# Optimization experiments

Hardware: AMD Instinct MI355X
Metric: run time of the kernel (lower is better)

Reference implementation:

```python
import jax, jax.numpy as jnp
import numpy as np

N_NODES = 100000
N_EDGES = 320000
N_GRAPHS = 4096
HID = 256
NUM_FEAT = 28


def setup_inputs() -> dict:
    key = jax.random.key(0)
    ks = jax.random.split(key, 20)
    inp = {}
    inp['x'] = jax.random.normal(ks[0], (N_NODES, NUM_FEAT), dtype=jnp.float32)
    inp['edge_index'] = jax.random.randint(ks[1], (2, N_EDGES), 0, N_NODES, dtype=jnp.int64)
    inp['batch'] = jnp.sort(jax.random.randint(ks[2], (N_NODES,), 0, N_GRAPHS, dtype=jnp.int64))
    def lin(k, out_d, in_d, scale=None):
        s = scale if scale is not None else 1.0 / np.sqrt(in_d)
        return jax.random.uniform(k, (out_d, in_d), jnp.float32, -s, s)
    # GraphConv layer l: W_rel (neighbor aggregate), b_rel, W_root (self)
    dims = [(HID, NUM_FEAT), (HID, HID), (HID, HID), (HID, HID)]
    for i, (o, d) in enumerate(dims, 1):
        inp[f'W{i}_rel'] = lin(ks[2 + 3 * i], o, d)
        inp[f'b{i}_rel'] = jnp.zeros((o,), jnp.float32)
        inp[f'W{i}_root'] = lin(ks[3 + 3 * i], o, d)
    inp['fc1_w'] = lin(ks[15], HID, 4 * HID)
    inp['fc1_b'] = jnp.zeros((HID,), jnp.float32)
    inp['fc2_w'] = lin(ks[16], HID, HID)
    inp['fc2_b'] = jnp.zeros((HID,), jnp.float32)
    inp['fc3_w'] = lin(ks[17], HID, HID)
    inp['fc3_b'] = jnp.zeros((HID,), jnp.float32)
    inp['fc4_w'] = lin(ks[18], 1, HID)
    inp['fc4_b'] = jnp.zeros((1,), jnp.float32)
    return inp


def _graph_conv(x, src, dst, W_rel, b_rel, W_root):
    # PyG GraphConv (aggr='add'): out = lin_rel(sum_{j->i} x_j) + lin_root(x_i)
    agg = jax.ops.segment_sum(x[src], dst, num_segments=N_NODES)  # [N, d]
    return agg @ W_rel.T + b_rel + x @ W_root.T


def reference(x, edge_index, batch,
              W1_rel, b1_rel, W1_root, W2_rel, b2_rel, W2_root,
              W3_rel, b3_rel, W3_root, W4_rel, b4_rel, W4_root,
              fc1_w, fc1_b, fc2_w, fc2_b, fc3_w, fc3_b, fc4_w, fc4_b):
    src, dst = edge_index[0], edge_index[1]
    x1 = jax.nn.relu(_graph_conv(x, src, dst, W1_rel, b1_rel, W1_root))
    x2 = jax.nn.relu(_graph_conv(x1, src, dst, W2_rel, b2_rel, W2_root))
    x3 = jax.nn.relu(_graph_conv(x2, src, dst, W3_rel, b3_rel, W3_root))
    x4 = jax.nn.relu(_graph_conv(x3, src, dst, W4_rel, b4_rel, W4_root))
    h = jnp.concatenate([x1, x2, x3, x4], axis=-1)  # [N, 4*HID]
    # global mean pool over graphs
    sums = jax.ops.segment_sum(h, batch, num_segments=N_GRAPHS)  # [G, 4*HID]
    cnts = jax.ops.segment_sum(jnp.ones((h.shape[0],), h.dtype), batch, num_segments=N_GRAPHS)
    g = sums / jnp.maximum(cnts, 1.0)[:, None]
    g = jax.nn.relu(g @ fc1_w.T + fc1_b)
    g = jax.nn.relu(g @ fc2_w.T + fc2_b)
    g = jax.nn.relu(g @ fc3_w.T + fc3_b)
    out = g @ fc4_w.T + fc4_b  # [G, 1]
    return out.reshape(-1)
```

## Files before the change

### kernel.cpp

```cpp
#include <hip/hip_runtime.h>
#include <hip/hip_bf16.h>
#include <cstdio>

#define HID 256

using short8  = __attribute__((ext_vector_type(8))) short;
using floatx4 = __attribute__((ext_vector_type(4))) float;

typedef const unsigned int __attribute__((address_space(1)))* as1_cuintp;
typedef unsigned int __attribute__((address_space(3)))* as3_uintp;

__device__ inline unsigned short bf16_rn(float x) {
    unsigned u = __float_as_uint(x);
    return (unsigned short)((u + 0x7FFFu + ((u >> 16) & 1u)) >> 16);
}
__device__ inline float bf2f(unsigned short u) {
    return __uint_as_float(((unsigned)u) << 16);
}

__global__ void marker_k(float* __restrict__ out, int n, float v) {
    int i = blockIdx.x * blockDim.x + threadIdx.x;
    if (i < n) out[i] = v;
}

__global__ void detect64_k(const unsigned* __restrict__ eiw, int E,
                           const unsigned* __restrict__ bw, int Nh,
                           int* __restrict__ any_nonzero) {
    int total = E + Nh;
    unsigned loc = 0;
    for (int i = blockIdx.x * blockDim.x + threadIdx.x; i < total;
         i += gridDim.x * blockDim.x) {
        loc |= (i < E) ? eiw[2 * i + 1] : bw[2 * (i - E) + 1];
    }
    if (loc) atomicOr(any_nonzero, 1);
}

__global__ void norm_idx_k(const int* __restrict__ src, int* __restrict__ dst,
                           int n, const int* __restrict__ any_nonzero) {
    int is64 = (any_nonzero[0] == 0);
    for (int i = blockIdx.x * blockDim.x + threadIdx.x; i < n;
         i += gridDim.x * blockDim.x) {
        dst[i] = is64 ? src[2 * i] : src[i];
    }
}

__global__ void pool_bounds_k(const int* __restrict__ batch, int N, int G,
                              int* __restrict__ starts) {
    int g = blockIdx.x * blockDim.x + threadIdx.x;
    if (g > G) return;
    int lo = 0, hi = N;
    while (lo < hi) {
        int mid = (lo + hi) >> 1;
        if (batch[mid] < g) lo = mid + 1; else hi = mid;
    }
    starts[g] = lo;
}

__global__ void deg_count_k(const int* __restrict__ ei, int E, int N,
                            int* __restrict__ deg) {
    int e = blockIdx.x * blockDim.x + threadIdx.x;
    if (e >= E) return;
    int s = ei[e];
    int d = ei[E + e];
    if ((unsigned)s >= (unsigned)N || (unsigned)d >= (unsigned)N) return;
    atomicAdd(&deg[d], 1);
}

#define SCAN_BLK 256

__global__ __launch_bounds__(SCAN_BLK) void scan_a_k(const int* __restrict__ deg,
                                                     int* __restrict__ bsum, int N) {
    __shared__ int red[SCAN_BLK];
    int i = blockIdx.x * SCAN_BLK + threadIdx.x;
    int v = (i < N) ? deg[i] : 0;
    red[threadIdx.x] = v;
    __syncthreads();
#pragma unroll
    for (int off = SCAN_BLK / 2; off > 0; off >>= 1) {
        if (threadIdx.x < off) red[threadIdx.x] += red[threadIdx.x + off];
        __syncthreads();
    }
    if (threadIdx.x == 0) bsum[blockIdx.x] = red[0];
}

__global__ __launch_bounds__(1024) void scan_b_k(int* __restrict__ bsum, int nb) {
    __shared__ int tsum[1024];
    int t = threadIdx.x;
    int v = (t < nb) ? bsum[t] : 0;
    tsum[t] = v;
    __syncthreads();
    for (int off = 1; off < 1024; off <<= 1) {
        int u = (t >= off) ? tsum[t - off] : 0;
        __syncthreads();
        tsum[t] += u;
        __syncthreads();
    }
    if (t < nb) bsum[t] = tsum[t] - v;
}

__global__ __launch_bounds__(SCAN_BLK) void scan_c_k(const int* __restrict__ deg,
                                                     const int* __restrict__ bsum,
                                                     int* __restrict__ row_ptr, int N) {
    __shared__ int tsum[SCAN_BLK];
    int t = threadIdx.x;
    int i = blockIdx.x * SCAN_BLK + t;
    int v = (i < N) ? deg[i] : 0;
    tsum[t] = v;
    __syncthreads();
    for (int off = 1; off < SCAN_BLK; off <<= 1) {
        int u = (t >= off) ? tsum[t - off] : 0;
        __syncthreads();
        tsum[t] += u;
        __syncthreads();
    }
    if (i <= N) row_ptr[i] = tsum[t] - v + bsum[blockIdx.x];
}

__global__ __launch_bounds__(1024) void scan_rowptr_k(const int* __restrict__ deg,
                                                      int* __restrict__ row_ptr, int N) {
    __shared__ int tsum[1024];
    int t = threadIdx.x;
    int chunk = (N + 1023) / 1024;
    int lo = t * chunk;
    int hi = min(lo + chunk, N);
    int s = 0;
    for (int i = lo; i < hi; i++) s += deg[i];
    tsum[t] = s;
    __syncthreads();
    for (int off = 1; off < 1024; off <<= 1) {
        int v = (t >= off) ? tsum[t - off] : 0;
        __syncthreads();
        tsum[t] += v;
        __syncthreads();
    }
    int run = (t == 0) ? 0 : tsum[t - 1];
    for (int i = lo; i < hi; i++) { row_ptr[i] = run; run += deg[i]; }
    if (hi >= N && lo <= N) row_ptr[N] = run;
}

__global__ void fill_csr_k(const int* __restrict__ ei, int E, int N,
                           const int* __restrict__ row_ptr, int* __restrict__ cursor,
                           int* __restrict__ esrc) {
    int e = blockIdx.x * blockDim.x + threadIdx.x;
    if (e >= E) return;
    int s = ei[e];
    int d = ei[E + e];
    if ((unsigned)s >= (unsigned)N || (unsigned)d >= (unsigned)N) return;
    int pos = atomicAdd(&cursor[d], 1);
    esrc[row_ptr[d] + pos] = s;
}

__global__ void gather28_k(const float* __restrict__ x, const int* __restrict__ row_ptr,
                           const int* __restrict__ esrc, float* __restrict__ Q28, int N) {
    int gid = blockIdx.x * blockDim.x + threadIdx.x;
    int node = gid >> 5;
    if (node >= N) return;
    int lane = gid & 31;
    if (lane >= 28) return;
    int s = row_ptr[node], e = row_ptr[node + 1];
    float acc = 0.f;
    for (int i = s; i < e; i++) {
        int src = esrc[i];
        acc += x[(size_t)src * 28 + lane];
    }
    Q28[(size_t)node * 28 + lane] = acc;
}

__global__ void gather256_k(const float* __restrict__ P, const int* __restrict__ row_ptr,
                            const int* __restrict__ esrc, float* __restrict__ Q, int N) {
    int gid = blockIdx.x * blockDim.x + threadIdx.x;
    int node = gid >> 6;
    if (node >= N) return;
    int lane = gid & 63;
    int s = row_ptr[node], e = row_ptr[node + 1];
    float4 acc = make_float4(0.f, 0.f, 0.f, 0.f);
    for (int i = s; i < e; i++) {
        int src = esrc[i];
        float4 v = *(const float4*)(P + (size_t)src * HID + lane * 4);
        acc.x += v.x; acc.y += v.y; acc.z += v.z; acc.w += v.w;
    }
    *(float4*)(Q + (size_t)node * HID + lane * 4) = acc;
}

__global__ __launch_bounds__(256) void l1_fused_k(
    const float* __restrict__ x, const float* __restrict__ agg,
    const float* __restrict__ Wrel, const float* __restrict__ Wroot,
    const float* __restrict__ bias, float* __restrict__ out, int M) {
    __shared__ float As[64][28];
    __shared__ float Xs[64][28];
    int t = threadIdx.x;
    int n0 = blockIdx.x * 64;
    float wrel[28], wroot[28];
#pragma unroll
    for (int k = 0; k < 28; k++) {
        wrel[k]  = Wrel[t * 28 + k];
        wroot[k] = Wroot[t * 28 + k];
    }
    float b = bias[t];
    for (int idx = t; idx < 64 * 28; idx += 256) {
        int r = idx / 28;
        int c = idx - r * 28;
        int gr = n0 + r;
        As[r][c] = (gr < M) ? agg[(size_t)gr * 28 + c] : 0.f;
        Xs[r][c] = (gr < M) ? x[(size_t)gr * 28 + c] : 0.f;
    }
    __syncthreads();
    int nmax = min(64, M - n0);
    for (int n = 0; n < nmax; n++) {
        float acc = b;
#pragma unroll
        for (int k4 = 0; k4 < 28; k4 += 4) {
            float4 a  = *(const float4*)&As[n][k4];
            float4 xx = *(const float4*)&Xs[n][k4];
            acc += a.x * wrel[k4] + a.y * wrel[k4 + 1] + a.z * wrel[k4 + 2] + a.w * wrel[k4 + 3];
            acc += xx.x * wroot[k4] + xx.y * wroot[k4 + 1] + xx.z * wroot[k4 + 2] + xx.w * wroot[k4 + 3];
        }
        out[(size_t)(n0 + n) * HID + t] = fmaxf(acc, 0.f);
    }
}

__global__ void wsplit6_k(const float* W0, const float* W1, const float* W2,
                          const float* W3, const float* W4, const float* W5,
                          unsigned short* __restrict__ out_hl, int n) {
    int i = blockIdx.x * blockDim.x + threadIdx.x;
    if (i >= n) return;
    const float* W = (blockIdx.y == 0) ? W0 : (blockIdx.y == 1) ? W1 :
                     (blockIdx.y == 2) ? W2 : (blockIdx.y == 3) ? W3 :
                     (blockIdx.y == 4) ? W4 : W5;
    unsigned short* o = out_hl + (size_t)blockIdx.y * 131072;
    float a = W[i];
    unsigned short h = bf16_rn(a);
    unsigned short lo = bf16_rn(a - bf2f(h));
    int col = i >> 8;
    int k   = i & 255;
    int ch  = k >> 5;
    int sg  = (k >> 3) & 3;
    int e   = k & 7;
    int gp  = sg ^ ((col >> 1) & 3);
    size_t base = (size_t)ch * 16384 + (size_t)col * 32 + gp * 8 + e;
    o[base] = h;
    o[base + 8192] = lo;
}

#define LSTR 40

__global__ __launch_bounds__(256) void gemm_strip_mfma_k(
    const float* __restrict__ Q, const unsigned short* __restrict__ Wr_hl,
    float* __restrict__ P, const unsigned short* __restrict__ Wo_hl,
    const float* __restrict__ bias, int M) {
    __shared__ __attribute__((aligned(16))) unsigned short Ah[64 * LSTR];
    __shared__ __attribute__((aligned(16))) unsigned short Al[64 * LSTR];
    __shared__ __attribute__((aligned(16))) unsigned short Wbuf[8192];
    int t = threadIdx.x;
    int brow = blockIdx.x * 64;
    int w = t >> 6;
    int l = t & 63;

    floatx4 acc[4][4];
#pragma unroll
    for (int i = 0; i < 4; i++)
#pragma unroll
        for (int j = 0; j < 4; j++) acc[i][j] = (floatx4){0.f, 0.f, 0.f, 0.f};

    int srow = t >> 2;
    int sg   = t & 3;

    for (int ch = 0; ch < 16; ch++) {
        int phase2 = (ch >= 8);
        const float* A = phase2 ? P : Q;
        const unsigned short* Whl = phase2 ? Wo_hl : Wr_hl;
        int kbase = (ch & 7) * 32;

        {
            const char* wg = (const char*)(Whl + (size_t)(ch & 7) * 16384) + w * 4096;
            char* ld = (char*)Wbuf + w * 4096;
#pragma unroll
            for (int i = 0; i < 4; i++) {
                __builtin_amdgcn_global_load_lds(
                    (as1_cuintp)(const void*)(wg + i * 1024 + l * 16),
                    (as3_uintp)(void*)(ld + i * 1024),
                    16, 0, 0);
            }
        }
        {
            int gr = brow + srow;
            float v[8];
            if (gr < M) {
                float4 u0 = *(const float4*)(A + (size_t)gr * HID + kbase + sg * 8);
                float4 u1 = *(const float4*)(A + (size_t)gr * HID + kbase + sg * 8 + 4);
                v[0] = u0.x; v[1] = u0.y; v[2] = u0.z; v[3] = u0.w;
                v[4] = u1.x; v[5] = u1.y; v[6] = u1.z; v[7] = u1.w;
            } else {
#pragma unroll
                for (int j = 0; j < 8; j++) v[j] = 0.f;
            }
            union { unsigned short us[8]; short8 v8; } hh, ll;
#pragma unroll
            for (int j = 0; j < 8; j++) {
                unsigned short h = bf16_rn(v[j]);
                float hf = __uint_as_float(((unsigned)h) << 16);
                hh.us[j] = h;
                ll.us[j] = bf16_rn(v[j] - hf);
            }
            int base = srow * LSTR + sg * 8;
            *(short8*)(Ah + base) = hh.v8;
            *(short8*)(Al + base) = ll.v8;
        }
        __syncthreads();

        int frow = l & 15;
        int fg   = l >> 4;
        short8 ahf[4], alf[4], wf[4];
#pragma unroll
        for (int rt = 0; rt < 4; rt++) {
            int base = (rt * 16 + frow) * LSTR + fg * 8;
            ahf[rt] = *(short8*)(Ah + base);
            alf[rt] = *(short8*)(Al + base);
        }
#pragma unroll
        for (int ct = 0; ct < 4; ct++) {
            int col = w * 64 + ct * 16 + frow;
            int gp = fg ^ ((col >> 1) & 3);
            wf[ct] = *(short8*)(Wbuf + col * 32 + gp * 8);
        }
        asm volatile("s_waitcnt lgkmcnt(0)" ::: "memory");
        __builtin_amdgcn_sched_barrier(0);
        {
            const char* wg = (const char*)(Whl + (size_t)(ch & 7) * 16384 + 8192) + w * 4096;
            char* ld = (char*)Wbuf + w * 4096;
#pragma unroll
            for (int i = 0; i < 4; i++) {
                __builtin_amdgcn_global_load_lds(
                    (as1_cuintp)(const void*)(wg + i * 1024 + l * 16),
                    (as3_uintp)(void*)(ld + i * 1024),
                    16, 0, 0);
            }
        }
        __builtin_amdgcn_s_setprio(1);
#pragma unroll
        for (int rt = 0; rt < 4; rt++)
#pragma unroll
            for (int ct = 0; ct < 4; ct++) {
                acc[rt][ct] = __builtin_amdgcn_mfma_f32_16x16x32_bf16(
                    ahf[rt], wf[ct], acc[rt][ct], 0, 0, 0);
                acc[rt][ct] = __builtin_amdgcn_mfma_f32_16x16x32_bf16(
                    alf[rt], wf[ct], acc[rt][ct], 0, 0, 0);
            }
        __builtin_amdgcn_s_setprio(0);
        asm volatile("s_waitcnt vmcnt(0)" ::: "memory");
        __builtin_amdgcn_sched_barrier(0);
#pragma unroll
        for (int ct = 0; ct < 4; ct++) {
            int col = w * 64 + ct * 16 + frow;
            int gp = fg ^ ((col >> 1) & 3);
            wf[ct] = *(short8*)(Wbuf + col * 32 + gp * 8);
        }
        __builtin_amdgcn_s_setprio(1);
#pragma unroll
        for (int rt = 0; rt < 4; rt++)
#pragma unroll
            for (int ct = 0; ct < 4; ct++)
                acc[rt][ct] = __builtin_amdgcn_mfma_f32_16x16x32_bf16(
                    ahf[rt], wf[ct], acc[rt][ct], 0, 0, 0);
        __builtin_amdgcn_s_setprio(0);
        __syncthreads();
    }

#pragma unroll
    for (int ct = 0; ct < 4; ct++) {
        int gc = w * 64 + ct * 16 + (l & 15);
        float bs = bias[gc];
#pragma unroll
        for (int rt = 0; rt < 4; rt++) {
            floatx4 a = acc[rt][ct];
#pragma unroll
            for (int r = 0; r < 4; r++) {
                int gr = brow + rt * 16 + (l >> 4) * 4 + r;
                if (gr < M)
                    P[(size_t)gr * HID + gc] = fmaxf(a[r] + bs, 0.f);
            }
        }
    }
}

__global__ __launch_bounds__(256) void pool_slice_k(const float* __restrict__ xl,
                                                    const int* __restrict__ starts,
                                                    float* __restrict__ gslice, int N) {
    int g = blockIdx.x;
    int t = threadIdx.x;
    int s = starts[g], e = starts[g + 1];
    s = max(0, min(s, N));
    e = max(s, min(e, N));
    float a = 0.f;
    for (int n = s; n < e; n++) a += xl[(size_t)n * HID + t];
    float inv = 1.f / (float)max(e - s, 1);
    gslice[(size_t)g * 1024 + t] = a * inv;
}

#define BM 64
#define BN 64
#define BK 32
#define LP 68

__global__ __launch_bounds__(256) void gemm_dual_k(
    const float* __restrict__ A1, int lda1, const float* __restrict__ W1,
    const float* __restrict__ A2, int lda2, const float* __restrict__ W2,
    const float* __restrict__ bias, float* __restrict__ out, int ldout,
    int M, int K1, int K2, int relu) {
    __shared__ float As[BK][LP];
    __shared__ float Ws[BK][LP];
    int t = threadIdx.x;
    int brow = blockIdx.x * BM;
    int bcol = blockIdx.y * BN;
    int tx = t & 15, ty = t >> 4;
    float acc[4][4] = {{0.f}};
    int Ktot = K1 + K2;
    int srow = t >> 3;
    int sk4 = (t & 7) << 2;

    for (int kk = 0; kk < Ktot; kk += BK) {
        int phase2 = (kk >= K1);
        const float* A = phase2 ? A2 : A1;
        const float* W = phase2 ? W2 : W1;
        int lda = phase2 ? lda2 : lda1;
        int ldw = phase2 ? K2 : K1;
        int kbase = phase2 ? (kk - K1) : kk;
#pragma unroll
        for (int i = 0; i < 2; i++) {
            int r = srow + i * 32;
            int gr = brow + r;
            float4 v = make_float4(0.f, 0.f, 0.f, 0.f);
            if (gr < M) v = *(const float4*)(A + (size_t)gr * lda + kbase + sk4);
            As[sk4 + 0][r] = v.x; As[sk4 + 1][r] = v.y;
            As[sk4 + 2][r] = v.z; As[sk4 + 3][r] = v.w;
            float4 w = *(const float4*)(W + (size_t)(bcol + r) * ldw + kbase + sk4);
            Ws[sk4 + 0][r] = w.x; Ws[sk4 + 1][r] = w.y;
            Ws[sk4 + 2][r] = w.z; Ws[sk4 + 3][r] = w.w;
        }
        __syncthreads();
#pragma unroll
        for (int k = 0; k < BK; k++) {
            float4 a = *(const float4*)&As[k][ty << 2];
            float4 w = *(const float4*)&Ws[k][tx << 2];
            float av[4] = {a.x, a.y, a.z, a.w};
            float wv[4] = {w.x, w.y, w.z, w.w};
#pragma unroll
            for (int i = 0; i < 4; i++)
#pragma unroll
                for (int j = 0; j < 4; j++)
                    acc[i][j] = fmaf(av[i], wv[j], acc[i][j]);
        }
        __syncthreads();
    }
#pragma unroll
    for (int i = 0; i < 4; i++) {
        int gr = brow + (ty << 2) + i;
        if (gr >= M) continue;
#pragma unroll
        for (int j = 0; j < 4; j++) {
            int gc = bcol + (tx << 2) + j;
            float v = acc[i][j] + bias[gc];
            if (relu) v = fmaxf(v, 0.f);
            out[(size_t)gr * ldout + gc] = v;
        }
    }
}

__global__ void fc4_k(const float* __restrict__ in, const float* __restrict__ w,
                      const float* __restrict__ b, float* __restrict__ out, int M) {
    int gid = blockIdx.x * blockDim.x + threadIdx.x;
    int row = gid >> 6;
    if (row >= M) return;
    int lane = gid & 63;
    float4 v  = *(const float4*)(in + (size_t)row * HID + lane * 4);
    float4 ww = *(const float4*)(w + lane * 4);
    float acc = v.x * ww.x + v.y * ww.y + v.z * ww.z + v.w * ww.w;
#pragma unroll
    for (int off = 32; off; off >>= 1) acc += __shfl_down(acc, off);
    if (lane == 0) out[row] = acc + b[0];
}

extern "C" void kernel_launch(void* const* d_in, const int* in_sizes, int n_in,
                              void* d_out, int out_size, void* d_ws, size_t ws_size,
                              hipStream_t stream) {
    const int N = in_sizes[0] / 28;
    const int E = in_sizes[1] / 2;
    const int G = out_size;

    const float* x        = (const float*)d_in[0];
    const int*   ei_raw   = (const int*)d_in[1];
    const int*   b_raw    = (const int*)d_in[2];
    const float* W1_rel  = (const float*)d_in[3];
    const float* b1      = (const float*)d_in[4];
    const float* W1_root = (const float*)d_in[5];
    const float* W2_rel  = (const float*)d_in[6];
    const float* b2      = (const float*)d_in[7];
    const float* W2_root = (const float*)d_in[8];
    const float* W3_rel  = (const float*)d_in[9];
    const float* b3      = (const float*)d_in[10];
    const float* W3_root = (const float*)d_in[11];
    const float* W4_rel  = (const float*)d_in[12];
    const float* b4      = (const float*)d_in[13];
    const float* W4_root = (const float*)d_in[14];
    const float* fc1_w = (const float*)d_in[15];
    const float* fc1_b = (const float*)d_in[16];
    const float* fc2_w = (const float*)d_in[17];
    const float* fc2_b = (const float*)d_in[18];
    const float* fc3_w = (const float*)d_in[19];
    const float* fc3_b = (const float*)d_in[20];
    const float* fc4_w = (const float*)d_in[21];
    const float* fc4_b = (const float*)d_in[22];
    float* out = (float*)d_out;

    size_t fN  = (size_t)N * HID;
    size_t off_P      = 0;
    size_t off_Q      = off_P + fN;
    size_t off_gpool  = off_Q + fN;
    size_t off_t1     = off_gpool + (size_t)G * 1024;
    size_t off_t2     = off_t1 + (size_t)G * HID;
    size_t off_ei     = off_t2 + (size_t)G * HID;
    size_t off_batch  = off_ei + (size_t)2 * E;
    size_t off_starts = off_batch + (size_t)N;
    size_t off_flag   = off_starts + (size_t)(G + 1);
    size_t off_deg    = off_flag + 1;
    size_t off_cur    = off_deg + (size_t)N;
    size_t off_rowp   = off_cur + (size_t)N;
    size_t off_bsum   = off_rowp + (size_t)(N + 1);
    size_t off_esrc   = off_bsum + 1024;
    size_t off_wsplit = (off_esrc + (size_t)E + 3) & ~(size_t)3;
    size_t need = (off_wsplit + 393216 + 16) * 4;

    if (ws_size < need) {
        fprintf(stderr, "[kernel_launch] ws too small: ws=%zu need=%zu\n", ws_size, need);
        marker_k<<<(G + 255) / 256, 256, 0, stream>>>(out, G, (float)(ws_size >> 20));
        return;
    }

    float* wsf   = (float*)d_ws;
    float* P     = wsf + off_P;
    float* Q     = wsf + off_Q;
    float* gpool = wsf + off_gpool;
    float* t1    = wsf + off_t1;
    float* t2    = wsf + off_t2;
    int* nei     = (int*)(wsf + off_ei);
    int* nbatch  = (int*)(wsf + off_batch);
    int* starts  = (int*)(wsf + off_starts);
    int* flag    = (int*)(wsf + off_flag);
    int* deg     = (int*)(wsf + off_deg);
    int* cursor  = (int*)(wsf + off_cur);
    int* row_ptr = (int*)(wsf + off_rowp);
    int* bsum    = (int*)(wsf + off_bsum);
    int* esrc    = (int*)(wsf + off_esrc);
    unsigned short* wsplit = (unsigned short*)(wsf + off_wsplit);

    hipMemsetAsync(flag, 0, sizeof(int), stream);
    detect64_k<<<1024, 256, 0, stream>>>((const unsigned*)ei_raw, E,
                                         (const unsigned*)b_raw, N / 2, flag);
    norm_idx_k<<<1024, 256, 0, stream>>>(ei_raw, nei, 2 * E, flag);
    norm_idx_k<<<512, 256, 0, stream>>>(b_raw, nbatch, N, flag);

    pool_bounds_k<<<(G + 1 + 255) / 256, 256, 0, stream>>>(nbatch, N, G, starts);

    hipMemsetAsync(deg, 0, 2 * (size_t)N * sizeof(int), stream);
    deg_count_k<<<(E + 255) / 256, 256, 0, stream>>>(nei, E, N, deg);
    int nb = (N + 1 + SCAN_BLK - 1) / SCAN_BLK;
    if (nb <= 1024) {
        scan_a_k<<<nb, SCAN_BLK, 0, stream>>>(deg, bsum, N);
        scan_b_k<<<1, 1024, 0, stream>>>(bsum, nb);
        scan_c_k<<<nb, SCAN_BLK, 0, stream>>>(deg, bsum, row_ptr, N);
    } else {
        scan_rowptr_k<<<1, 1024, 0, stream>>>(deg, row_ptr, N);
    }
    fill_csr_k<<<(E + 255) / 256, 256, 0, stream>>>(nei, E, N, row_ptr, cursor, esrc);

    wsplit6_k<<<dim3((65536 + 255) / 256, 6), 256, 0, stream>>>(
        W2_rel, W2_root, W3_rel, W3_root, W4_rel, W4_root, wsplit, 65536);

    int nstrips = (N + 63) / 64;

    gather28_k<<<((size_t)N * 32 + 255) / 256, 256, 0, stream>>>(x, row_ptr, esrc, Q, N);
    l1_fused_k<<<nstrips, 256, 0, stream>>>(x, Q, W1_rel, W1_root, b1, P, N);
    pool_slice_k<<<G, 256, 0, stream>>>(P, starts, gpool + 0, N);

    const float* bb[3] = {b2, b3, b4};
    for (int l = 0; l < 3; l++) {
        gather256_k<<<((size_t)N * 64 + 255) / 256, 256, 0, stream>>>(P, row_ptr, esrc, Q, N);
        gemm_strip_mfma_k<<<nstrips, 256, 0, stream>>>(
            Q, wsplit + (size_t)(2 * l) * 131072,
            P, wsplit + (size_t)(2 * l + 1) * 131072, bb[l], N);
        pool_slice_k<<<G, 256, 0, stream>>>(P, starts, gpool + 256 * (l + 1), N);
    }

    dim3 gdimG(G / BM, HID / BN);
    gemm_dual_k<<<gdimG, 256, 0, stream>>>(gpool, 1024, fc1_w, nullptr, 0, nullptr,
                                           fc1_b, t1, HID, G, 1024, 0, 1);
    gemm_dual_k<<<gdimG, 256, 0, stream>>>(t1, HID, fc2_w, nullptr, 0, nullptr,
                                           fc2_b, t2, HID, G, HID, 0, 1);
    gemm_dual_k<<<gdimG, 256, 0, stream>>>(t2, HID, fc3_w, nullptr, 0, nullptr,
                                           fc3_b, t1, HID, G, HID, 0, 1);
    fc4_k<<<(G * 64 + 255) / 256, 256, 0, stream>>>(t1, fc4_w, fc4_b, out, G);
}
```

Measured before the change: 954.0 us.

## Run first GraphConv layer on MFMA with split-bf16 and padded 32-wide inputs

Replaces the scalar FMA first-layer kernel with an MFMA kernel that pads the 28-feature inputs and aggregates to 32 columns. It splits activations and weights into bf16 hi/lo parts (three products) to keep near-fp32 accuracy. It adds a padding kernel and a weight-split kernel, plus extra workspace for the padded arrays. The aim is to cut the compute and register-heavy scalar loop of the old layer-1 kernel, at the cost of an extra pass over x and slightly different rounding.

```diff
diff --git a/kernel.cpp b/kernel.cpp
--- a/kernel.cpp
+++ b/kernel.cpp
@@ -150,20 +150,29 @@
     esrc[row_ptr[d] + pos] = s;
 }
 
+__global__ void pad_x_k(const float* __restrict__ x, float* __restrict__ X32, int N) {
+    int i = blockIdx.x * blockDim.x + threadIdx.x;
+    if (i >= N * 32) return;
+    int node = i >> 5;
+    int lane = i & 31;
+    X32[i] = (lane < 28) ? x[(size_t)node * 28 + lane] : 0.f;
+}
+
 __global__ void gather28_k(const float* __restrict__ x, const int* __restrict__ row_ptr,
-                           const int* __restrict__ esrc, float* __restrict__ Q28, int N) {
+                           const int* __restrict__ esrc, float* __restrict__ Q32, int N) {
     int gid = blockIdx.x * blockDim.x + threadIdx.x;
     int node = gid >> 5;
     if (node >= N) return;
     int lane = gid & 31;
-    if (lane >= 28) return;
-    int s = row_ptr[node], e = row_ptr[node + 1];
     float acc = 0.f;
-    for (int i = s; i < e; i++) {
-        int src = esrc[i];
-        acc += x[(size_t)src * 28 + lane];
-    }
-    Q28[(size_t)node * 28 + lane] = acc;
+    if (lane < 28) {
+        int s = row_ptr[node], e = row_ptr[node + 1];
+        for (int i = s; i < e; i++) {
+            int src = esrc[i];
+            acc += x[(size_t)src * 28 + lane];
+        }
+    }
+    Q32[(size_t)node * 32 + lane] = acc;
 }
 
 __global__ void gather256_k(const float* __restrict__ P, const int* __restrict__ row_ptr,
@@ -180,43 +189,6 @@
         acc.x += v.x; acc.y += v.y; acc.z += v.z; acc.w += v.w;
     }
     *(float4*)(Q + (size_t)node * HID + lane * 4) = acc;
-}
-
-__global__ __launch_bounds__(256) void l1_fused_k(
-    const float* __restrict__ x, const float* __restrict__ agg,
-    const float* __restrict__ Wrel, const float* __restrict__ Wroot,
-    const float* __restrict__ bias, float* __restrict__ out, int M) {
-    __shared__ float As[64][28];
-    __shared__ float Xs[64][28];
-    int t = threadIdx.x;
-    int n0 = blockIdx.x * 64;
-    float wrel[28], wroot[28];
-#pragma unroll
-    for (int k = 0; k < 28; k++) {
-        wrel[k]  = Wrel[t * 28 + k];
-        wroot[k] = Wroot[t * 28 + k];
-    }
-    float b = bias[t];
-    for (int idx = t; idx < 64 * 28; idx += 256) {
-        int r = idx / 28;
-        int c = idx - r * 28;
-        int gr = n0 + r;
-        As[r][c] = (gr < M) ? agg[(size_t)gr * 28 + c] : 0.f;
-        Xs[r][c] = (gr < M) ? x[(size_t)gr * 28 + c] : 0.f;
-    }
-    __syncthreads();
-    int nmax = min(64, M - n0);
-    for (int n = 0; n < nmax; n++) {
-        float acc = b;
-#pragma unroll
-        for (int k4 = 0; k4 < 28; k4 += 4) {
-            float4 a  = *(const float4*)&As[n][k4];
-            float4 xx = *(const float4*)&Xs[n][k4];
-            acc += a.x * wrel[k4] + a.y * wrel[k4 + 1] + a.z * wrel[k4 + 2] + a.w * wrel[k4 + 3];
-            acc += xx.x * wroot[k4] + xx.y * wroot[k4 + 1] + xx.z * wroot[k4 + 2] + xx.w * wroot[k4 + 3];
-        }
-        out[(size_t)(n0 + n) * HID + t] = fmaxf(acc, 0.f);
-    }
 }
 
 __global__ void wsplit6_k(const float* W0, const float* W1, const float* W2,
@@ -242,7 +214,165 @@
     o[base + 8192] = lo;
 }
 
+__global__ void wsplit1_k(const float* __restrict__ W0, const float* __restrict__ W1,
+                          unsigned short* __restrict__ o) {
+    int i = blockIdx.x * blockDim.x + threadIdx.x;
+    if (i >= 2 * 8192) return;
+    int m   = i >> 13;
+    int r   = i & 8191;
+    int col = r >> 5;
+    int k   = r & 31;
+    const float* W = m ? W1 : W0;
+    float a = (k < 28) ? W[col * 28 + k] : 0.f;
+    unsigned short h = bf16_rn(a);
+    unsigned short lo = bf16_rn(a - bf2f(h));
+    int sg = (k >> 3) & 3;
+    int e  = k & 7;
+    int gp = sg ^ ((col >> 1) & 3);
+    size_t base = (size_t)m * 16384 + (size_t)col * 32 + gp * 8 + e;
+    o[base] = h;
+    o[base + 8192] = lo;
+}
+
 #define LSTR 40
+
+__global__ __launch_bounds__(256) void l1_mfma_k(
+    const float* __restrict__ Q32, const unsigned short* __restrict__ Wrel_hl,
+    const float* __restrict__ X32, const unsigned short* __restrict__ Wroot_hl,
+    const float* __restrict__ bias, float* __restrict__ P, int M) {
+    __shared__ __attribute__((aligned(16))) unsigned short Ah[64 * LSTR];
+    __shared__ __attribute__((aligned(16))) unsigned short Al[64 * LSTR];
+    __shared__ __attribute__((aligned(16))) unsigned short Wbuf[8192];
+    int t = threadIdx.x;
+    int brow = blockIdx.x * 64;
+    int w = t >> 6;
+    int l = t & 63;
+
+    floatx4 acc[4][4];
+#pragma unroll
+    for (int i = 0; i < 4; i++)
+#pragma unroll
+        for (int j = 0; j < 4; j++) acc[i][j] = (floatx4){0.f, 0.f, 0.f, 0.f};
+
+    int srow = t >> 2;
+    int sg   = t & 3;
+
+#pragma unroll
+    for (int ch = 0; ch < 2; ch++) {
+        const float* A = ch ? X32 : Q32;
+        const unsigned short* Whl = ch ? Wroot_hl : Wrel_hl;
+
+        {
+            const char* wg = (const char*)Whl + w * 4096;
+            char* ld = (char*)Wbuf + w * 4096;
+#pragma unroll
+            for (int i = 0; i < 4; i++) {
+                __builtin_amdgcn_global_load_lds(
+                    (as1_cuintp)(const void*)(wg + i * 1024 + l * 16),
+                    (as3_uintp)(void*)(ld + i * 1024),
+                    16, 0, 0);
+            }
+        }
+        {
+            int gr = brow + srow;
+            float v[8];
+            if (gr < M) {
+                float4 u0 = *(const float4*)(A + (size_t)gr * 32 + sg * 8);
+                float4 u1 = *(const float4*)(A + (size_t)gr * 32 + sg * 8 + 4);
+                v[0] = u0.x; v[1] = u0.y; v[2] = u0.z; v[3] = u0.w;
+                v[4] = u1.x; v[5] = u1.y; v[6] = u1.z; v[7] = u1.w;
+            } else {
+#pragma unroll
+                for (int j = 0; j < 8; j++) v[j] = 0.f;
+            }
+            union { unsigned short us[8]; short8 v8; } hh, ll;
+#pragma unroll
+            for (int j = 0; j < 8; j++) {
+                unsigned short h = bf16_rn(v[j]);
+                float hf = bf2f(h);
+                hh.us[j] = h;
+                ll.us[j] = bf16_rn(v[j] - hf);
+            }
+            int base = srow * LSTR + sg * 8;
+            *(short8*)(Ah + base) = hh.v8;
+            *(short8*)(Al + base) = ll.v8;
+        }
+        __syncthreads();
+
+        int frow = l & 15;
+        int fg   = l >> 4;
+        short8 ahf[4], alf[4], wf[4];
+#pragma unroll
+        for (int rt = 0; rt < 4; rt++) {
+            int base = (rt * 16 + frow) * LSTR + fg * 8;
+            ahf[rt] = *(short8*)(Ah + base);
+            alf[rt] = *(short8*)(Al + base);
+        }
+#pragma unroll
+        for (int ct = 0; ct < 4; ct++) {
+            int col = w * 64 + ct * 16 + frow;
+            int gp = fg ^ ((col >> 1) & 3);
+            wf[ct] = *(short8*)(Wbuf + col * 32 + gp * 8);
+        }
+        asm volatile("s_waitcnt lgkmcnt(0)" ::: "memory");
+        __builtin_amdgcn_sched_barrier(0);
+        {
+            const char* wg = (const char*)(Whl + 8192) + w * 4096;
+            char* ld = (char*)Wbuf + w * 4096;
+#pragma unroll
+            for (int i = 0; i < 4; i++) {
+                __builtin_amdgcn_global_load_lds(
+                    (as1_cuintp)(const void*)(wg + i * 1024 + l * 16),
+                    (as3_uintp)(void*)(ld + i * 1024),
+                    16, 0, 0);
+            }
+        }
+        __builtin_amdgcn_s_setprio(1);
+#pragma unroll
+        for (int rt = 0; rt < 4; rt++)
+#pragma unroll
+            for (int ct = 0; ct < 4; ct++) {
+                acc[rt][ct] = __builtin_amdgcn_mfma_f32_16x16x32_bf16(
+                    ahf[rt], wf[ct], acc[rt][ct], 0, 0, 0);
+                acc[rt][ct] = __builtin_amdgcn_mfma_f32_16x16x32_bf16(
+                    alf[rt], wf[ct], acc[rt][ct], 0, 0, 0);
+            }
+        __builtin_amdgcn_s_setprio(0);
+        asm volatile("s_waitcnt vmcnt(0)" ::: "memory");
+        __builtin_amdgcn_sched_barrier(0);
+#pragma unroll
+        for (int ct = 0; ct < 4; ct++) {
+            int col = w * 64 + ct * 16 + frow;
+            int gp = fg ^ ((col >> 1) & 3);
+            wf[ct] = *(short8*)(Wbuf + col * 32 + gp * 8);
+        }
+        __builtin_amdgcn_s_setprio(1);
+#pragma unroll
+        for (int rt = 0; rt < 4; rt++)
+#pragma unroll
+            for (int ct = 0; ct < 4; ct++)
+                acc[rt][ct] = __builtin_amdgcn_mfma_f32_16x16x32_bf16(
+                    ahf[rt], wf[ct], acc[rt][ct], 0, 0, 0);
+        __builtin_amdgcn_s_setprio(0);
+        __syncthreads();
+    }
+
+#pragma unroll
+    for (int ct = 0; ct < 4; ct++) {
+        int gc = w * 64 + ct * 16 + (l & 15);
+        float bs = bias[gc];
+#pragma unroll
+        for (int rt = 0; rt < 4; rt++) {
+            floatx4 a = acc[rt][ct];
+#pragma unroll
+            for (int r = 0; r < 4; r++) {
+                int gr = brow + rt * 16 + (l >> 4) * 4 + r;
+                if (gr < M)
+                    P[(size_t)gr * HID + gc] = fmaxf(a[r] + bs, 0.f);
+            }
+        }
+    }
+}
 
 __global__ __launch_bounds__(256) void gemm_strip_mfma_k(
     const float* __restrict__ Q, const unsigned short* __restrict__ Wr_hl,
@@ -298,7 +428,7 @@
 #pragma unroll
             for (int j = 0; j < 8; j++) {
                 unsigned short h = bf16_rn(v[j]);
-                float hf = __uint_as_float(((unsigned)h) << 16);
+                float hf = bf2f(h);
                 hh.us[j] = h;
                 ll.us[j] = bf16_rn(v[j] - hf);
             }
@@ -528,7 +658,10 @@
     size_t off_bsum   = off_rowp + (size_t)(N + 1);
     size_t off_esrc   = off_bsum + 1024;
     size_t off_wsplit = (off_esrc + (size_t)E + 3) & ~(size_t)3;
-    size_t need = (off_wsplit + 393216 + 16) * 4;
+    size_t off_w1     = off_wsplit + 393216;
+    size_t off_X32    = (off_w1 + 16384 + 3) & ~(size_t)3;
+    size_t off_Q32    = off_X32 + (size_t)N * 32;
+    size_t need = (off_Q32 + (size_t)N * 32 + 16) * 4;
 
     if (ws_size < need) {
         fprintf(stderr, "[kernel_launch] ws too small: ws=%zu need=%zu\n", ws_size, need);
@@ -552,6 +685,9 @@
     int* bsum    = (int*)(wsf + off_bsum);
     int* esrc    = (int*)(wsf + off_esrc);
     unsigned short* wsplit = (unsigned short*)(wsf + off_wsplit);
+    unsigned short* w1split = (unsigned short*)(wsf + off_w1);
+    float* X32   = wsf + off_X32;
+    float* Q32   = wsf + off_Q32;
 
     hipMemsetAsync(flag, 0, sizeof(int), stream);
     detect64_k<<<1024, 256, 0, stream>>>((const unsigned*)ei_raw, E,
@@ -575,11 +711,13 @@
 
     wsplit6_k<<<dim3((65536 + 255) / 256, 6), 256, 0, stream>>>(
         W2_rel, W2_root, W3_rel, W3_root, W4_rel, W4_root, wsplit, 65536);
+    wsplit1_k<<<(2 * 8192 + 255) / 256, 256, 0, stream>>>(W1_rel, W1_root, w1split);
 
     int nstrips = (N + 63) / 64;
 
-    gather28_k<<<((size_t)N * 32 + 255) / 256, 256, 0, stream>>>(x, row_ptr, esrc, Q, N);
-    l1_fused_k<<<nstrips, 256, 0, stream>>>(x, Q, W1_rel, W1_root, b1, P, N);
+    pad_x_k<<<((size_t)N * 32 + 255) / 256, 256, 0, stream>>>(x, X32, N);
+    gather28_k<<<((size_t)N * 32 + 255) / 256, 256, 0, stream>>>(x, row_ptr, esrc, Q32, N);
+    l1_mfma_k<<<nstrips, 256, 0, stream>>>(Q32, w1split, X32, w1split + 16384, b1, P, N);
     pool_slice_k<<<G, 256, 0, stream>>>(P, starts, gpool + 0, N);
 
     const float* bb[3] = {b2, b3, b4};
```

Result: faster. 895.9 us (-6.1%).
